# Kernel tuning notes

Hardware: AMD Instinct MI355X
Metric: run time of the kernel (lower is better)

Reference implementation:

```python
import jax, jax.numpy as jnp
import numpy as np

NBATCH, NATOM, NEIGH = 16, 512, 64
NTYPE, NWAVE, NIPSIN, NORBIT = 4, 8, 3, 128
CUTOFF = 5.0
NPAIR = NATOM * NEIGH  # neighbor pairs per configuration


def _make_index_para(nipsin):
    # [0, 1,1,1, 2,...(9 times)] -> angular-order label per channel
    parts = [np.zeros(1, np.int32)]
    for i in range(1, nipsin):
        parts.append(np.full(3 ** i, i, np.int32))
    return jnp.asarray(np.concatenate(parts))


def setup_inputs() -> dict:
    key = jax.random.key(0)
    ks = jax.random.split(key, 10)
    cart = jax.random.uniform(ks[0], (NBATCH, NATOM, 3), jnp.float32) * 6.0
    numatoms = jnp.full((NBATCH,), NATOM, dtype=jnp.int32)
    species = jax.random.randint(ks[1], (NBATCH * NATOM,), 0, NTYPE).astype(jnp.int32)
    atom_index = jax.random.randint(ks[2], (2, NBATCH, NPAIR), 0, NATOM).astype(jnp.int32)
    shifts = jnp.zeros((NBATCH, NPAIR, 3), jnp.float32)  # all pairs valid (pass >-1e10 check)
    # learned parameters / buffers
    rs = jnp.tile(jnp.linspace(0.5, 4.0, NWAVE, dtype=jnp.float32)[None, :], (NTYPE, 1))
    inta = -(jax.random.uniform(ks[3], (NTYPE, NWAVE), jnp.float32) * 0.9 + 0.1)
    params = jnp.ones((NTYPE, NWAVE), jnp.float32) / float(NEIGH)
    hyper = jax.random.normal(ks[4], (1, NIPSIN, NWAVE, NORBIT), jnp.float32) * (1.0 / np.sqrt(NWAVE))
    index_para = _make_index_para(NIPSIN)
    return {"cart": cart, "numatoms": numatoms, "species": species,
            "atom_index": atom_index, "shifts": shifts,
            "rs": rs, "inta": inta, "params": params, "hyper": hyper,
            "index_para": index_para, "cutoff": CUTOFF}


def _angular(dist_vec, f_cut, nipsin):
    # dist_vec: [N,3], f_cut: [N] -> [L, N] with L = 1 + 3 + ... + 3^(nipsin-1)
    dv = dist_vec.T  # [3, N]
    orb = f_cut[None, :]
    parts = [orb]
    for _ in range(1, nipsin):
        orb = (orb[:, None, :] * dv[None, :, :]).reshape(-1, dv.shape[1])
        parts.append(orb)
    return jnp.concatenate(parts, axis=0)


def reference(cart, numatoms, species, atom_index, shifts, rs, inta, params, hyper, index_para, cutoff):
    nbatch, natom, _ = cart.shape
    totnatom = nbatch * natom
    cart_ = cart.reshape(totnatom, 3)
    # offset per-config neighbor indices to global atom ids
    offs = (jnp.arange(nbatch, dtype=atom_index.dtype) * natom)[None, :, None]
    idx12 = (atom_index + offs).reshape(2, -1)  # [2, Npairs]
    dist_vec = cart_[idx12[0]] - cart_[idx12[1]] + shifts.reshape(-1, 3)  # [Npairs,3]
    distances = jnp.linalg.norm(dist_vec, axis=-1)  # [Npairs]
    sp_j = species[idx12[1]]
    f_cut = jnp.square(0.5 * jnp.cos(distances * (jnp.pi / cutoff)) + 0.5)
    # per-pair gaussian radial basis, gathered by neighbor element type
    radial = jnp.exp(inta[sp_j] * jnp.square(distances[:, None] - rs[sp_j]))  # [Npairs, nwave]
    ang = _angular(dist_vec, f_cut, NIPSIN)  # [L, Npairs]
    orbital = ang.T[:, :, None] * radial[:, None, :]  # [Npairs, L, nwave]
    orb_coeff = params[species]  # [totnatom, nwave] (all species >= 0)
    # iteration 0 (ocmod_list is empty, so no refinement loop)
    worb = orbital * orb_coeff[idx12[1]][:, None, :]  # [Npairs, L, nwave]
    sum_worb = jax.ops.segment_sum(worb, idx12[0], num_segments=totnatom)  # [totnatom, L, nwave]
    hp = hyper[0][index_para]  # [L, nwave, norbit]
    hw = jnp.einsum('ijk,jkm->ijm', sum_worb, hp)  # [totnatom, L, norbit]
    density = jnp.sum(jnp.square(hw), axis=1)  # [totnatom, norbit]
    return density
```

## Files before the change

### kernel.cpp

```cpp
#include <hip/hip_runtime.h>
#include <hip/hip_bf16.h>

#define NBATCH  16
#define NATOM   512
#define NEIGH   64
#define NPAIR   (NATOM * NEIGH)
#define TOTPAIR (NBATCH * NPAIR)
#define TOTATOM (NBATCH * NATOM)
#define NTYPE   4
#define NWAVE   8
#define NL      13
#define NORBIT  128
#define CAP     128
#define CAPP    130


__global__ __launch_bounds__(1024) void fill_kernel(
    const int* __restrict__ atom_index,
    int*       __restrict__ count,
    unsigned short* __restrict__ bucket)
{
    const int b   = blockIdx.x;
    const int tid = threadIdx.x;

    __shared__ int s_cnt[NATOM];
    if (tid < NATOM) s_cnt[tid] = 0;
    __syncthreads();

    const int pbase = b * NPAIR;
#pragma unroll
    for (int it = 0; it < NPAIR / 1024; ++it) {
        int pl = it * 1024 + tid;
        int il = atom_index[pbase + pl];
        int slot = atomicAdd(&s_cnt[il], 1);
        if (slot < CAP)
            bucket[((size_t)(b * NATOM + il)) * CAP + slot] = (unsigned short)pl;
    }
    __syncthreads();

    if (tid < NATOM) count[b * NATOM + tid] = s_cnt[tid];
}

__global__ __launch_bounds__(128) void gather_kernel(
    const float* __restrict__ cart,
    const int*   __restrict__ species,
    const int*   __restrict__ atom_index,
    const float* __restrict__ shifts,
    const float* __restrict__ rs,
    const float* __restrict__ inta,
    const float* __restrict__ params,
    const float* __restrict__ cutoff_p,
    const int*   __restrict__ count,
    const unsigned short* __restrict__ bucket,
    const float* __restrict__ hyper,
    float*       __restrict__ out)
{
    const int i    = blockIdx.x;
    const int b    = i >> 9;
    const int base = b << 9;
    const int tid  = threadIdx.x;

    __shared__ float s_a [NL][CAPP];
    __shared__ float s_rp[NWAVE][CAPP];
    __shared__ float s_d [CAP];
    __shared__ int   s_sp[CAP];
    __shared__ float s_S [NL * NWAVE];
    __shared__ float s_tab[3 * NTYPE * NWAVE];

    if (tid < NTYPE * NWAVE) {
        s_tab[tid]                   = rs[tid];
        s_tab[NTYPE * NWAVE + tid]   = inta[tid];
        s_tab[2 * NTYPE * NWAVE + tid] = params[tid];
    }

    const int cnt0 = count[i];
    const int cnt  = cnt0 < CAP ? cnt0 : CAP;

    const float cx  = cart[3 * i + 0];
    const float cy  = cart[3 * i + 1];
    const float cz  = cart[3 * i + 2];
    const float pic = 3.14159265358979323846f / cutoff_p[0];

    for (int k = tid; k < cnt; k += 128) {
        int p = (b << 15) | (int)bucket[(size_t)i * CAP + k];
        int j = atom_index[TOTPAIR + p] + base;

        float dx = cx - cart[3 * j + 0] + shifts[3 * p + 0];
        float dy = cy - cart[3 * j + 1] + shifts[3 * p + 1];
        float dz = cz - cart[3 * j + 2] + shifts[3 * p + 2];
        float d  = sqrtf(dx * dx + dy * dy + dz * dz);

        float c  = 0.5f * __cosf(d * pic) + 0.5f;
        float fc = c * c;

        s_d[k]  = d;
        s_sp[k] = species[j];

        float a1 = fc * dx, a2 = fc * dy, a3 = fc * dz;
        s_a[0][k]  = fc;
        s_a[1][k]  = a1;       s_a[2][k]  = a2;       s_a[3][k]  = a3;
        s_a[4][k]  = a1 * dx;  s_a[5][k]  = a1 * dy;  s_a[6][k]  = a1 * dz;
        s_a[7][k]  = a2 * dx;  s_a[8][k]  = a2 * dy;  s_a[9][k]  = a2 * dz;
        s_a[10][k] = a3 * dx;  s_a[11][k] = a3 * dy;  s_a[12][k] = a3 * dz;
    }
    __syncthreads();

    for (int t = tid; t < cnt * NWAVE; t += 128) {
        int k = t >> 3, w = t & 7;
        int sp = s_sp[k];
        float d  = s_d[k];
        float tt = d - s_tab[sp * NWAVE + w];
        s_rp[w][k] = __expf(s_tab[NTYPE * NWAVE + sp * NWAVE + w] * tt * tt)
                   * s_tab[2 * NTYPE * NWAVE + sp * NWAVE + w];
    }
    __syncthreads();

    if (tid < NL * NWAVE) {
        int l = tid >> 3, w = tid & 7;
        float S = 0.0f;
        int k = 0;
        for (; k + 1 < cnt; k += 2) {
            float2 av = *(const float2*)&s_a[l][k];
            float2 rv = *(const float2*)&s_rp[w][k];
            S += av.x * rv.x;
            S += av.y * rv.y;
        }
        if (k < cnt) S += s_a[l][k] * s_rp[w][k];
        s_S[tid] = S;
    }
    __syncthreads();

    const int m = tid;
    float acc = 0.0f;
#pragma unroll
    for (int l = 0; l < NL; ++l) {
        int ip = (l == 0) ? 0 : ((l < 4) ? 1 : 2);
        const float* hp = hyper + (size_t)ip * (NWAVE * NORBIT) + m;
        float h = 0.0f;
#pragma unroll
        for (int w = 0; w < NWAVE; ++w)
            h += s_S[l * NWAVE + w] * hp[w * NORBIT];
        acc += h * h;
    }
    out[(size_t)i * NORBIT + m] = acc;
}

extern "C" void kernel_launch(void* const* d_in, const int* in_sizes, int n_in,
                              void* d_out, int out_size, void* d_ws, size_t ws_size,
                              hipStream_t stream) {
    const float* cart       = (const float*)d_in[0];
    const int*   species    = (const int*)  d_in[2];
    const int*   atom_index = (const int*)  d_in[3];
    const float* shifts     = (const float*)d_in[4];
    const float* rs         = (const float*)d_in[5];
    const float* inta       = (const float*)d_in[6];
    const float* params     = (const float*)d_in[7];
    const float* hyper      = (const float*)d_in[8];
    const float* cutoff_p   = (const float*)d_in[10];

    int* count = (int*)d_ws;
    unsigned short* bucket =
        (unsigned short*)((char*)d_ws + TOTATOM * sizeof(int));
    float* out = (float*)d_out;

    fill_kernel<<<NBATCH, 1024, 0, stream>>>(atom_index, count, bucket);

    gather_kernel<<<TOTATOM, 128, 0, stream>>>(
        cart, species, atom_index, shifts, rs, inta, params, cutoff_p,
        count, bucket, hyper, out);
}
```

Baseline: 133.8 us.

## Split neighbor bucketing across sub-blocks and fuse radial basis into pair loop

The fill kernel used to run only 16 blocks, one per configuration. It now launches 128 blocks, each bucketing one eighth of a configuration's pairs into its own sub-bucket with a separate count. The gather kernel computes prefix offsets over the sub-buckets and maps each pair slot back to its sub-bucket. It also computes the Gaussian radial terms in the same loop as the angular terms, which removes one shared-memory pass and one barrier. The trade-offs are more count reads, a per-pair search over the offsets, and a per-sub-bucket cap of 40 that could drop pairs if neighbors cluster.

```diff
diff --git a/kernel.cpp b/kernel.cpp
--- a/kernel.cpp
+++ b/kernel.cpp
@@ -13,32 +13,36 @@
 #define NORBIT  128
 #define CAP     128
 #define CAPP    130
+#define NSUB    8
+#define SUBCAP  40
+#define PAIRS_PER_SUB (NPAIR / NSUB)
 
 
-__global__ __launch_bounds__(1024) void fill_kernel(
+__global__ __launch_bounds__(512) void fill_kernel(
     const int* __restrict__ atom_index,
     int*       __restrict__ count,
     unsigned short* __restrict__ bucket)
 {
-    const int b   = blockIdx.x;
+    const int b   = blockIdx.x >> 3;
+    const int s   = blockIdx.x & 7;
     const int tid = threadIdx.x;
 
     __shared__ int s_cnt[NATOM];
-    if (tid < NATOM) s_cnt[tid] = 0;
+    s_cnt[tid] = 0;
     __syncthreads();
 
-    const int pbase = b * NPAIR;
 #pragma unroll
-    for (int it = 0; it < NPAIR / 1024; ++it) {
-        int pl = it * 1024 + tid;
-        int il = atom_index[pbase + pl];
+    for (int it = 0; it < PAIRS_PER_SUB / 512; ++it) {
+        int pl = s * PAIRS_PER_SUB + it * 512 + tid;
+        int il = atom_index[b * NPAIR + pl];
         int slot = atomicAdd(&s_cnt[il], 1);
-        if (slot < CAP)
-            bucket[((size_t)(b * NATOM + il)) * CAP + slot] = (unsigned short)pl;
+        if (slot < SUBCAP)
+            bucket[((size_t)((b * NATOM + il) * NSUB + s)) * SUBCAP + slot] =
+                (unsigned short)pl;
     }
     __syncthreads();
 
-    if (tid < NATOM) count[b * NATOM + tid] = s_cnt[tid];
+    count[(b * NATOM + tid) * NSUB + s] = s_cnt[tid];
 }
 
 __global__ __launch_bounds__(128) void gather_kernel(
@@ -62,28 +66,44 @@
 
     __shared__ float s_a [NL][CAPP];
     __shared__ float s_rp[NWAVE][CAPP];
-    __shared__ float s_d [CAP];
-    __shared__ int   s_sp[CAP];
     __shared__ float s_S [NL * NWAVE];
     __shared__ float s_tab[3 * NTYPE * NWAVE];
+    __shared__ int   s_off[NSUB + 1];
 
     if (tid < NTYPE * NWAVE) {
-        s_tab[tid]                   = rs[tid];
-        s_tab[NTYPE * NWAVE + tid]   = inta[tid];
+        s_tab[tid]                     = rs[tid];
+        s_tab[NTYPE * NWAVE + tid]     = inta[tid];
         s_tab[2 * NTYPE * NWAVE + tid] = params[tid];
     }
+    if (tid == 0) {
+        int o = 0;
+#pragma unroll
+        for (int s2 = 0; s2 < NSUB; ++s2) {
+            s_off[s2] = o;
+            int c = count[i * NSUB + s2];
+            o += (c < SUBCAP ? c : SUBCAP);
+        }
+        s_off[NSUB] = o;
+    }
+    __syncthreads();
 
-    const int cnt0 = count[i];
-    const int cnt  = cnt0 < CAP ? cnt0 : CAP;
+    int total = s_off[NSUB];
+    if (total > CAP) total = CAP;
 
     const float cx  = cart[3 * i + 0];
     const float cy  = cart[3 * i + 1];
     const float cz  = cart[3 * i + 2];
     const float pic = 3.14159265358979323846f / cutoff_p[0];
 
-    for (int k = tid; k < cnt; k += 128) {
-        int p = (b << 15) | (int)bucket[(size_t)i * CAP + k];
-        int j = atom_index[TOTPAIR + p] + base;
+    for (int k = tid; k < total; k += 128) {
+        int s2 = 0;
+#pragma unroll
+        for (int t = 1; t < NSUB; ++t)
+            if (k >= s_off[t]) s2 = t;
+        int local = k - s_off[s2];
+        int pl = (int)bucket[((size_t)(i * NSUB + s2)) * SUBCAP + local];
+        int p  = (b << 15) | pl;
+        int j  = atom_index[TOTPAIR + p] + base;
 
         float dx = cx - cart[3 * j + 0] + shifts[3 * p + 0];
         float dy = cy - cart[3 * j + 1] + shifts[3 * p + 1];
@@ -93,25 +113,20 @@
         float c  = 0.5f * __cosf(d * pic) + 0.5f;
         float fc = c * c;
 
-        s_d[k]  = d;
-        s_sp[k] = species[j];
-
         float a1 = fc * dx, a2 = fc * dy, a3 = fc * dz;
         s_a[0][k]  = fc;
         s_a[1][k]  = a1;       s_a[2][k]  = a2;       s_a[3][k]  = a3;
         s_a[4][k]  = a1 * dx;  s_a[5][k]  = a1 * dy;  s_a[6][k]  = a1 * dz;
         s_a[7][k]  = a2 * dx;  s_a[8][k]  = a2 * dy;  s_a[9][k]  = a2 * dz;
         s_a[10][k] = a3 * dx;  s_a[11][k] = a3 * dy;  s_a[12][k] = a3 * dz;
-    }
-    __syncthreads();
 
-    for (int t = tid; t < cnt * NWAVE; t += 128) {
-        int k = t >> 3, w = t & 7;
-        int sp = s_sp[k];
-        float d  = s_d[k];
-        float tt = d - s_tab[sp * NWAVE + w];
-        s_rp[w][k] = __expf(s_tab[NTYPE * NWAVE + sp * NWAVE + w] * tt * tt)
-                   * s_tab[2 * NTYPE * NWAVE + sp * NWAVE + w];
+        int sp = species[j];
+#pragma unroll
+        for (int w = 0; w < NWAVE; ++w) {
+            float tt = d - s_tab[sp * NWAVE + w];
+            s_rp[w][k] = __expf(s_tab[NTYPE * NWAVE + sp * NWAVE + w] * tt * tt)
+                       * s_tab[2 * NTYPE * NWAVE + sp * NWAVE + w];
+        }
     }
     __syncthreads();
 
@@ -119,13 +134,13 @@
         int l = tid >> 3, w = tid & 7;
         float S = 0.0f;
         int k = 0;
-        for (; k + 1 < cnt; k += 2) {
+        for (; k + 1 < total; k += 2) {
             float2 av = *(const float2*)&s_a[l][k];
             float2 rv = *(const float2*)&s_rp[w][k];
             S += av.x * rv.x;
             S += av.y * rv.y;
         }
-        if (k < cnt) S += s_a[l][k] * s_rp[w][k];
+        if (k < total) S += s_a[l][k] * s_rp[w][k];
         s_S[tid] = S;
     }
     __syncthreads();
@@ -160,10 +175,10 @@
 
     int* count = (int*)d_ws;
     unsigned short* bucket =
-        (unsigned short*)((char*)d_ws + TOTATOM * sizeof(int));
+        (unsigned short*)((char*)d_ws + (size_t)TOTATOM * NSUB * sizeof(int));
     float* out = (float*)d_out;
 
-    fill_kernel<<<NBATCH, 1024, 0, stream>>>(atom_index, count, bucket);
+    fill_kernel<<<NBATCH * NSUB, 512, 0, stream>>>(atom_index, count, bucket);
 
     gather_kernel<<<TOTATOM, 128, 0, stream>>>(
         cart, species, atom_index, shifts, rs, inta, params, cutoff_p,
```

After: 107.9 us. -19.4%, faster.
